# Optimization experiments

Measured on AMD Instinct MI355X. Metric: run time of the kernel, lower is better.

## Reference

```python
import jax, jax.numpy as jnp
import numpy as np

B, F_DIM, T = 16, 256, 4096
L = 128           # latent_dim
CF = 2            # combineVQ_frames
K = 2             # codebook_num
M = 1024          # codebook_size (n_embeddings)
D = L * CF // K   # codebook_dim = 128
TC = T // CF      # combined frames
ALPHA = -5.0      # distance->logit scale
TAU = 2.0         # max_temp (curr_temp at init)


def setup_inputs() -> dict:
    key = jax.random.key(0)
    k1, k2, k3, k4, k5 = jax.random.split(key, 5)
    inputs = jax.random.normal(k1, (B, F_DIM, T, 1), dtype=jnp.float32)
    # xavier-ish scaled 1x1 conv weights
    w1 = jax.random.normal(k2, (L, F_DIM), dtype=jnp.float32) * (2.0 / (L + F_DIM)) ** 0.5
    w2 = jax.random.normal(k3, (F_DIM, L), dtype=jnp.float32) * (2.0 / (L + F_DIM)) ** 0.5
    # codebooks init uniform(-1, 1) as in nn.init.uniform_(a=-1, b=1)
    codebooks = jax.random.uniform(k4, (K, M, D), dtype=jnp.float32, minval=-1.0, maxval=1.0)
    # gumbel noise that torch's F.gumbel_softmax would sample internally
    u = jax.random.uniform(k5, (K, B * TC, M), dtype=jnp.float32, minval=1e-7, maxval=1.0 - 1e-7)
    gumbels = -jnp.log(-jnp.log(u))
    return {"inputs": inputs, "w1": w1, "w2": w2, "codebooks": codebooks, "gumbels": gumbels}


def _vq_layer(vq_in, emb, g):
    # vq_in: [B, TC, D], emb: [M, D], g: [B*TC, M]
    xf = vq_in.reshape(-1, D)  # [N, D]
    dist = (jnp.sum(emb ** 2, axis=1)[None, :]
            + jnp.sum(xf ** 2, axis=1, keepdims=True)
            - 2.0 * (xf @ emb.T))                      # [N, M]
    logits = ALPHA * dist
    # straight-through hard gumbel-softmax (training path of F.gumbel_softmax(hard=True))
    y_soft = jax.nn.softmax((logits + g) / TAU, axis=-1)
    idx = jnp.argmax(y_soft, axis=-1)                  # [N]
    y_hard = jax.nn.one_hot(idx, M, dtype=y_soft.dtype)
    y = y_hard + y_soft - jax.lax.stop_gradient(y_soft)
    q = y @ emb                                        # [N, D] dequantize
    return q.reshape(B, TC, D), idx.reshape(B, TC)


def reference(inputs, w1, w2, codebooks, gumbels):
    # conv1x1_1: [B, F, T, 1] -> [B, L, T, 1]; then squeeze(-1).permute(0,2,1) -> [B, T, L]
    x = jnp.einsum('bfto,lf->btl', inputs, w1)         # [B, T, L]
    # combine frames and split channels across codebooks
    xc = x.reshape(B, TC, CF, L)                       # [B, TC, CF, L]
    chunks = jnp.split(xc, K, axis=-1)                 # K x [B, TC, CF, L/K]
    quants, inds = [], []
    for i in range(K):
        vq_in = chunks[i].reshape(B, TC, D)            # CF*(L/K) == D
        q, idx = _vq_layer(vq_in, codebooks[i], gumbels[i])
        quants.append(q.reshape(B, TC, CF, L // K))
        inds.append(idx)
    vq_feat = jnp.concatenate(quants, axis=-1).reshape(B, T, L)  # [B, T, L]
    # conv1x1_2: back to [B, F, T, 1]
    out = jnp.einsum('btl,fl->bft', vq_feat, w2)[..., None]
    quant_inds = jnp.stack(inds, axis=-1)              # [B, TC, K]
    return out, vq_feat, quant_inds
```

## Files before the change

kernel.cpp:

```cpp
#include <hip/hip_runtime.h>
#include <cstdint>
#include <cmath>

#define B_ 16
#define F_ 256
#define T_ 4096
#define L_ 128
#define TC_ 2048
#define D_ 128
#define M_ 1024
#define NROWS_ 32768

#define PAD 132


__global__ __launch_bounds__(256) void gemm1_kernel(
    const float* __restrict__ in, const float* __restrict__ w1,
    float* __restrict__ x) {
  __shared__ float As[32 * PAD];
  __shared__ float Bs[32 * PAD];
  const int tid = threadIdx.x;
  const int blk = blockIdx.x;
  const int b = blk >> 5;
  const int t0 = (blk & 31) << 7;
  const int tm = tid & 15;
  const int tr = tid >> 4;
  const float* inb = in + (size_t)b * F_ * T_;
  float acc[8][8];
#pragma unroll
  for (int i = 0; i < 8; ++i)
#pragma unroll
    for (int j = 0; j < 8; ++j) acc[i][j] = 0.f;

  for (int f0 = 0; f0 < F_; f0 += 32) {
#pragma unroll
    for (int it = 0; it < 4; ++it) {
      int e = tid + it * 256;
      int ff = e >> 5, q = e & 31;
      float4 v = *(const float4*)(inb + (size_t)(f0 + ff) * T_ + t0 + q * 4);
      *(float4*)(&As[ff * PAD + q * 4]) = v;
    }
#pragma unroll
    for (int it = 0; it < 4; ++it) {
      int e = tid + it * 256;
      int l = e >> 3, q = e & 7;
      float4 v = *(const float4*)(w1 + l * F_ + f0 + q * 4);
      Bs[(q * 4 + 0) * PAD + l] = v.x;
      Bs[(q * 4 + 1) * PAD + l] = v.y;
      Bs[(q * 4 + 2) * PAD + l] = v.z;
      Bs[(q * 4 + 3) * PAD + l] = v.w;
    }
    __syncthreads();
#pragma unroll
    for (int ff = 0; ff < 32; ++ff) {
      float a[8], w[8];
      *(float4*)&a[0] = *(const float4*)&As[ff * PAD + tr * 8];
      *(float4*)&a[4] = *(const float4*)&As[ff * PAD + tr * 8 + 4];
      *(float4*)&w[0] = *(const float4*)&Bs[ff * PAD + 4 * tm];
      *(float4*)&w[4] = *(const float4*)&Bs[ff * PAD + 64 + 4 * tm];
#pragma unroll
      for (int i = 0; i < 8; ++i)
#pragma unroll
        for (int j = 0; j < 8; ++j) acc[i][j] = fmaf(a[i], w[j], acc[i][j]);
    }
    __syncthreads();
  }
  float* xb = x + ((size_t)b * T_ + t0) * L_;
#pragma unroll
  for (int i = 0; i < 8; ++i) {
    float* dst = xb + (size_t)(tr * 8 + i) * L_;
    *(float4*)(dst + 4 * tm) = make_float4(acc[i][0], acc[i][1], acc[i][2], acc[i][3]);
    *(float4*)(dst + 64 + 4 * tm) = make_float4(acc[i][4], acc[i][5], acc[i][6], acc[i][7]);
  }
}

__global__ __launch_bounds__(256) void c2_kernel(const float* __restrict__ cbs,
                                                 float* __restrict__ c2) {
  int m = blockIdx.x * 256 + threadIdx.x;
  const float* row = cbs + (size_t)m * D_;
  float s = 0.f;
#pragma unroll
  for (int d = 0; d < D_; d += 4) {
    float4 v = *(const float4*)(row + d);
    s += v.x * v.x;
    s += v.y * v.y;
    s += v.z * v.z;
    s += v.w * v.w;
  }
  c2[m] = s;
}

__global__ __launch_bounds__(256) void vq_kernel(
    const float* __restrict__ x, const float* __restrict__ cbs,
    const float* __restrict__ gum, const float* __restrict__ c2,
    float* __restrict__ vq_feat, float* __restrict__ qinds) {
  __shared__ float smem[2 * 32 * PAD];
  __shared__ int widx[128];
  float* Xs = smem;
  float* Es = smem + 32 * PAD;
  const int tid = threadIdx.x;
  const int blk = blockIdx.x;
  const int cb = blk >> 8;
  const int n0 = (blk & 255) << 7;
  const int tm = tid & 15;
  const int tr = tid >> 4;
  const float* cbp = cbs + (size_t)cb * M_ * D_;
  const float* gp = gum + (size_t)cb * NROWS_ * M_;
  const float* c2p = c2 + cb * M_;

  float best[8];
  int bidx[8];
#pragma unroll
  for (int i = 0; i < 8; ++i) {
    best[i] = -INFINITY;
    bidx[i] = 0;
  }

  for (int mt = 0; mt < 8; ++mt) {
    const int m0 = mt << 7;
    float acc[8][8];
#pragma unroll
    for (int i = 0; i < 8; ++i)
#pragma unroll
      for (int j = 0; j < 8; ++j) acc[i][j] = 0.f;

    for (int d0 = 0; d0 < D_; d0 += 32) {
      const int cf = d0 >> 6;
      const int j0 = d0 & 63;
#pragma unroll
      for (int it = 0; it < 4; ++it) {
        int e = tid + it * 256;
        int r = e >> 3, q = e & 7;
        int n = n0 + r;
        int bb = n >> 11, tc = n & 2047;
        const float* src =
            x + ((size_t)bb * T_ + 2 * tc + cf) * L_ + cb * 64 + j0 + q * 4;
        float4 v = *(const float4*)src;
        Xs[(q * 4 + 0) * PAD + r] = v.x;
        Xs[(q * 4 + 1) * PAD + r] = v.y;
        Xs[(q * 4 + 2) * PAD + r] = v.z;
        Xs[(q * 4 + 3) * PAD + r] = v.w;
      }
#pragma unroll
      for (int it = 0; it < 4; ++it) {
        int e = tid + it * 256;
        int mm = e >> 3, q = e & 7;
        const float* src = cbp + (size_t)(m0 + mm) * D_ + d0 + q * 4;
        float4 v = *(const float4*)src;
        Es[(q * 4 + 0) * PAD + mm] = v.x;
        Es[(q * 4 + 1) * PAD + mm] = v.y;
        Es[(q * 4 + 2) * PAD + mm] = v.z;
        Es[(q * 4 + 3) * PAD + mm] = v.w;
      }
      __syncthreads();
#pragma unroll
      for (int dd = 0; dd < 32; ++dd) {
        float a[8], w[8];
        *(float4*)&a[0] = *(const float4*)&Xs[dd * PAD + tr * 8];
        *(float4*)&a[4] = *(const float4*)&Xs[dd * PAD + tr * 8 + 4];
        *(float4*)&w[0] = *(const float4*)&Es[dd * PAD + 4 * tm];
        *(float4*)&w[4] = *(const float4*)&Es[dd * PAD + 64 + 4 * tm];
#pragma unroll
        for (int i = 0; i < 8; ++i)
#pragma unroll
          for (int j = 0; j < 8; ++j) acc[i][j] = fmaf(a[i], w[j], acc[i][j]);
      }
      __syncthreads();
    }
    float cc[8];
    *(float4*)&cc[0] = *(const float4*)(c2p + m0 + 4 * tm);
    *(float4*)&cc[4] = *(const float4*)(c2p + m0 + 64 + 4 * tm);
#pragma unroll
    for (int i = 0; i < 8; ++i) {
      int n = n0 + tr * 8 + i;
      const float* grow = gp + (size_t)n * M_ + m0;
      float g[8];
      *(float4*)&g[0] = *(const float4*)(grow + 4 * tm);
      *(float4*)&g[4] = *(const float4*)(grow + 64 + 4 * tm);
#pragma unroll
      for (int j = 0; j < 8; ++j) {
        float dist = cc[j] - 2.f * acc[i][j];
        float sc = fmaf(-5.f, dist, g[j]);
        if (sc > best[i]) {
          best[i] = sc;
          bidx[i] = m0 + ((j >> 2) ? (64 + 4 * tm + (j & 3)) : (4 * tm + (j & 3)));
        }
      }
    }
  }
  float* rbest = smem;
  int* ridx = (int*)(smem + 128 * 17);
#pragma unroll
  for (int i = 0; i < 8; ++i) {
    rbest[(tr * 8 + i) * 17 + tm] = best[i];
    ridx[(tr * 8 + i) * 17 + tm] = bidx[i];
  }
  __syncthreads();
  if (tid < 128) {
    float bv = rbest[tid * 17];
    int bi = ridx[tid * 17];
#pragma unroll
    for (int k = 1; k < 16; ++k) {
      float v = rbest[tid * 17 + k];
      int ii = ridx[tid * 17 + k];
      if (v > bv || (v == bv && ii < bi)) {
        bv = v;
        bi = ii;
      }
    }
    widx[tid] = bi;
    int n = n0 + tid;
    qinds[(size_t)n * 2 + cb] = (float)bi;
  }
  __syncthreads();
  const int jj = (tid & 15) * 4;
  for (int seg = tid >> 4; seg < 256; seg += 16) {
    int r = seg >> 1, cf = seg & 1;
    int wi = widx[r];
    float4 v = *(const float4*)(cbp + (size_t)wi * D_ + cf * 64 + jj);
    int n = n0 + r;
    int bb = n >> 11, tc = n & 2047;
    float* dst = vq_feat + ((size_t)bb * T_ + 2 * tc + cf) * L_ + cb * 64 + jj;
    *(float4*)dst = v;
  }
}

__global__ __launch_bounds__(256) void gemm2_kernel(
    const float* __restrict__ vq, const float* __restrict__ w2,
    float* __restrict__ out) {
  __shared__ float As[32 * PAD];
  __shared__ float Bs[32 * PAD];
  const int tid = threadIdx.x;
  const int blk = blockIdx.x;
  const int b = blk >> 6;
  const int rest = blk & 63;
  const int t0 = (rest >> 1) << 7;
  const int f0 = (rest & 1) << 7;
  const int tm = tid & 15;
  const int tr = tid >> 4;
  const float* vb = vq + (size_t)b * T_ * L_;
  float acc[8][8];
#pragma unroll
  for (int i = 0; i < 8; ++i)
#pragma unroll
    for (int j = 0; j < 8; ++j) acc[i][j] = 0.f;

  for (int l0 = 0; l0 < L_; l0 += 32) {
#pragma unroll
    for (int it = 0; it < 4; ++it) {
      int e = tid + it * 256;
      int t = e >> 3, q = e & 7;
      float4 v = *(const float4*)(vb + (size_t)(t0 + t) * L_ + l0 + q * 4);
      As[(q * 4 + 0) * PAD + t] = v.x;
      As[(q * 4 + 1) * PAD + t] = v.y;
      As[(q * 4 + 2) * PAD + t] = v.z;
      As[(q * 4 + 3) * PAD + t] = v.w;
    }
#pragma unroll
    for (int it = 0; it < 4; ++it) {
      int e = tid + it * 256;
      int f = e >> 3, q = e & 7;
      float4 v = *(const float4*)(w2 + (size_t)(f0 + f) * L_ + l0 + q * 4);
      Bs[(q * 4 + 0) * PAD + f] = v.x;
      Bs[(q * 4 + 1) * PAD + f] = v.y;
      Bs[(q * 4 + 2) * PAD + f] = v.z;
      Bs[(q * 4 + 3) * PAD + f] = v.w;
    }
    __syncthreads();
#pragma unroll
    for (int dd = 0; dd < 32; ++dd) {
      float a[8], w[8];
      *(float4*)&a[0] = *(const float4*)&As[dd * PAD + tr * 8];
      *(float4*)&a[4] = *(const float4*)&As[dd * PAD + tr * 8 + 4];
      *(float4*)&w[0] = *(const float4*)&Bs[dd * PAD + 4 * tm];
      *(float4*)&w[4] = *(const float4*)&Bs[dd * PAD + 64 + 4 * tm];
#pragma unroll
      for (int i = 0; i < 8; ++i)
#pragma unroll
        for (int j = 0; j < 8; ++j) acc[i][j] = fmaf(a[i], w[j], acc[i][j]);
    }
    __syncthreads();
  }
  float* ob = out + ((size_t)b * F_ + f0) * T_ + t0;
#pragma unroll
  for (int jj = 0; jj < 4; ++jj) {
    float* dst = ob + (size_t)(4 * tm + jj) * T_ + tr * 8;
    *(float4*)dst = make_float4(acc[0][jj], acc[1][jj], acc[2][jj], acc[3][jj]);
    *(float4*)(dst + 4) = make_float4(acc[4][jj], acc[5][jj], acc[6][jj], acc[7][jj]);
    float* dst2 = ob + (size_t)(64 + 4 * tm + jj) * T_ + tr * 8;
    *(float4*)dst2 =
        make_float4(acc[0][4 + jj], acc[1][4 + jj], acc[2][4 + jj], acc[3][4 + jj]);
    *(float4*)(dst2 + 4) =
        make_float4(acc[4][4 + jj], acc[5][4 + jj], acc[6][4 + jj], acc[7][4 + jj]);
  }
}

extern "C" void kernel_launch(void* const* d_in, const int* in_sizes, int n_in,
                              void* d_out, int out_size, void* d_ws,
                              size_t ws_size, hipStream_t stream) {
  const float* in = (const float*)d_in[0];
  const float* w1 = (const float*)d_in[1];
  const float* w2 = (const float*)d_in[2];
  const float* cbs = (const float*)d_in[3];
  const float* gum = (const float*)d_in[4];
  float* out = (float*)d_out;
  float* vq_feat = out + 16777216;
  float* qinds = out + 25165824;
  float* x = out;
  float* c2 = out + 8388608;

  hipLaunchKernelGGL(gemm1_kernel, dim3(512), dim3(256), 0, stream, in, w1, x);
  hipLaunchKernelGGL(c2_kernel, dim3(8), dim3(256), 0, stream, cbs, c2);
  hipLaunchKernelGGL(vq_kernel, dim3(512), dim3(256), 0, stream, x, cbs, gum,
                     c2, vq_feat, qinds);
  hipLaunchKernelGGL(gemm2_kernel, dim3(1024), dim3(256), 0, stream, vq_feat,
                     w2, out);
}
```

Before: 684.6 us.

## Halve row tiles to 64 and keep full X tile resident in shared memory

All three GEMM-style kernels move from 128-row to 64-row tiles with 4x8 per-thread accumulators, which doubles the grid size and cuts register pressure so more waves can be resident on the 256 CUs. The VQ kernel also loads its entire 64x128 X slice into shared memory once, instead of reloading X for every codebook tile. The cost is lower arithmetic intensity per thread and more repeated loads of codebook tiles across blocks, since each block now covers fewer rows.

```diff
diff --git a/kernel.cpp b/kernel.cpp
--- a/kernel.cpp
+++ b/kernel.cpp
@@ -11,55 +11,54 @@
 #define M_ 1024
 #define NROWS_ 32768
 
-#define PAD 132
+#define PADE 132
 
 
 __global__ __launch_bounds__(256) void gemm1_kernel(
     const float* __restrict__ in, const float* __restrict__ w1,
     float* __restrict__ x) {
-  __shared__ float As[32 * PAD];
-  __shared__ float Bs[32 * PAD];
+  __shared__ float As[32 * 64];
+  __shared__ float Bs[32 * PADE];
   const int tid = threadIdx.x;
   const int blk = blockIdx.x;
-  const int b = blk >> 5;
-  const int t0 = (blk & 31) << 7;
+  const int b = blk >> 6;
+  const int t0 = (blk & 63) << 6;
   const int tm = tid & 15;
   const int tr = tid >> 4;
   const float* inb = in + (size_t)b * F_ * T_;
-  float acc[8][8];
-#pragma unroll
-  for (int i = 0; i < 8; ++i)
+  float acc[4][8];
+#pragma unroll
+  for (int i = 0; i < 4; ++i)
 #pragma unroll
     for (int j = 0; j < 8; ++j) acc[i][j] = 0.f;
 
   for (int f0 = 0; f0 < F_; f0 += 32) {
 #pragma unroll
-    for (int it = 0; it < 4; ++it) {
+    for (int it = 0; it < 2; ++it) {
       int e = tid + it * 256;
-      int ff = e >> 5, q = e & 31;
+      int ff = e >> 4, q = e & 15;
       float4 v = *(const float4*)(inb + (size_t)(f0 + ff) * T_ + t0 + q * 4);
-      *(float4*)(&As[ff * PAD + q * 4]) = v;
+      *(float4*)(&As[ff * 64 + q * 4]) = v;
     }
 #pragma unroll
     for (int it = 0; it < 4; ++it) {
       int e = tid + it * 256;
       int l = e >> 3, q = e & 7;
       float4 v = *(const float4*)(w1 + l * F_ + f0 + q * 4);
-      Bs[(q * 4 + 0) * PAD + l] = v.x;
-      Bs[(q * 4 + 1) * PAD + l] = v.y;
-      Bs[(q * 4 + 2) * PAD + l] = v.z;
-      Bs[(q * 4 + 3) * PAD + l] = v.w;
+      Bs[(q * 4 + 0) * PADE + l] = v.x;
+      Bs[(q * 4 + 1) * PADE + l] = v.y;
+      Bs[(q * 4 + 2) * PADE + l] = v.z;
+      Bs[(q * 4 + 3) * PADE + l] = v.w;
     }
     __syncthreads();
 #pragma unroll
     for (int ff = 0; ff < 32; ++ff) {
-      float a[8], w[8];
-      *(float4*)&a[0] = *(const float4*)&As[ff * PAD + tr * 8];
-      *(float4*)&a[4] = *(const float4*)&As[ff * PAD + tr * 8 + 4];
-      *(float4*)&w[0] = *(const float4*)&Bs[ff * PAD + 4 * tm];
-      *(float4*)&w[4] = *(const float4*)&Bs[ff * PAD + 64 + 4 * tm];
-#pragma unroll
-      for (int i = 0; i < 8; ++i)
+      float a[4], w[8];
+      *(float4*)&a[0] = *(const float4*)&As[ff * 64 + tr * 4];
+      *(float4*)&w[0] = *(const float4*)&Bs[ff * PADE + 4 * tm];
+      *(float4*)&w[4] = *(const float4*)&Bs[ff * PADE + 64 + 4 * tm];
+#pragma unroll
+      for (int i = 0; i < 4; ++i)
 #pragma unroll
         for (int j = 0; j < 8; ++j) acc[i][j] = fmaf(a[i], w[j], acc[i][j]);
     }
@@ -67,8 +66,8 @@
   }
   float* xb = x + ((size_t)b * T_ + t0) * L_;
 #pragma unroll
-  for (int i = 0; i < 8; ++i) {
-    float* dst = xb + (size_t)(tr * 8 + i) * L_;
+  for (int i = 0; i < 4; ++i) {
+    float* dst = xb + (size_t)(tr * 4 + i) * L_;
     *(float4*)(dst + 4 * tm) = make_float4(acc[i][0], acc[i][1], acc[i][2], acc[i][3]);
     *(float4*)(dst + 64 + 4 * tm) = make_float4(acc[i][4], acc[i][5], acc[i][6], acc[i][7]);
   }
@@ -94,74 +93,74 @@
     const float* __restrict__ x, const float* __restrict__ cbs,
     const float* __restrict__ gum, const float* __restrict__ c2,
     float* __restrict__ vq_feat, float* __restrict__ qinds) {
-  __shared__ float smem[2 * 32 * PAD];
-  __shared__ int widx[128];
+  __shared__ float smem[128 * 64 + 32 * PADE];
+  __shared__ int widx[64];
   float* Xs = smem;
-  float* Es = smem + 32 * PAD;
+  float* Es = smem + 128 * 64;
   const int tid = threadIdx.x;
   const int blk = blockIdx.x;
-  const int cb = blk >> 8;
-  const int n0 = (blk & 255) << 7;
+  const int cb = blk >> 9;
+  const int n0 = (blk & 511) << 6;
   const int tm = tid & 15;
   const int tr = tid >> 4;
   const float* cbp = cbs + (size_t)cb * M_ * D_;
   const float* gp = gum + (size_t)cb * NROWS_ * M_;
   const float* c2p = c2 + cb * M_;
 
-  float best[8];
-  int bidx[8];
-#pragma unroll
-  for (int i = 0; i < 8; ++i) {
+#pragma unroll
+  for (int it = 0; it < 8; ++it) {
+    int e = tid + it * 256;
+    int r = e & 63, qq = e >> 6;
+    int n = n0 + r;
+    int bb = n >> 11, tc = n & 2047;
+    int d = qq * 4;
+    int cf = d >> 6, j = d & 63;
+    const float* src = x + ((size_t)bb * T_ + 2 * tc + cf) * L_ + cb * 64 + j;
+    float4 v = *(const float4*)src;
+    Xs[(d + 0) * 64 + r] = v.x;
+    Xs[(d + 1) * 64 + r] = v.y;
+    Xs[(d + 2) * 64 + r] = v.z;
+    Xs[(d + 3) * 64 + r] = v.w;
+  }
+  __syncthreads();
+
+  float best[4];
+  int bidx[4];
+#pragma unroll
+  for (int i = 0; i < 4; ++i) {
     best[i] = -INFINITY;
     bidx[i] = 0;
   }
 
   for (int mt = 0; mt < 8; ++mt) {
     const int m0 = mt << 7;
-    float acc[8][8];
-#pragma unroll
-    for (int i = 0; i < 8; ++i)
+    float acc[4][8];
+#pragma unroll
+    for (int i = 0; i < 4; ++i)
 #pragma unroll
       for (int j = 0; j < 8; ++j) acc[i][j] = 0.f;
 
     for (int d0 = 0; d0 < D_; d0 += 32) {
-      const int cf = d0 >> 6;
-      const int j0 = d0 & 63;
-#pragma unroll
-      for (int it = 0; it < 4; ++it) {
-        int e = tid + it * 256;
-        int r = e >> 3, q = e & 7;
-        int n = n0 + r;
-        int bb = n >> 11, tc = n & 2047;
-        const float* src =
-            x + ((size_t)bb * T_ + 2 * tc + cf) * L_ + cb * 64 + j0 + q * 4;
-        float4 v = *(const float4*)src;
-        Xs[(q * 4 + 0) * PAD + r] = v.x;
-        Xs[(q * 4 + 1) * PAD + r] = v.y;
-        Xs[(q * 4 + 2) * PAD + r] = v.z;
-        Xs[(q * 4 + 3) * PAD + r] = v.w;
-      }
 #pragma unroll
       for (int it = 0; it < 4; ++it) {
         int e = tid + it * 256;
         int mm = e >> 3, q = e & 7;
         const float* src = cbp + (size_t)(m0 + mm) * D_ + d0 + q * 4;
         float4 v = *(const float4*)src;
-        Es[(q * 4 + 0) * PAD + mm] = v.x;
-        Es[(q * 4 + 1) * PAD + mm] = v.y;
-        Es[(q * 4 + 2) * PAD + mm] = v.z;
-        Es[(q * 4 + 3) * PAD + mm] = v.w;
+        Es[(q * 4 + 0) * PADE + mm] = v.x;
+        Es[(q * 4 + 1) * PADE + mm] = v.y;
+        Es[(q * 4 + 2) * PADE + mm] = v.z;
+        Es[(q * 4 + 3) * PADE + mm] = v.w;
       }
       __syncthreads();
 #pragma unroll
       for (int dd = 0; dd < 32; ++dd) {
-        float a[8], w[8];
-        *(float4*)&a[0] = *(const float4*)&Xs[dd * PAD + tr * 8];
-        *(float4*)&a[4] = *(const float4*)&Xs[dd * PAD + tr * 8 + 4];
-        *(float4*)&w[0] = *(const float4*)&Es[dd * PAD + 4 * tm];
-        *(float4*)&w[4] = *(const float4*)&Es[dd * PAD + 64 + 4 * tm];
-#pragma unroll
-        for (int i = 0; i < 8; ++i)
+        float a[4], w[8];
+        *(float4*)&a[0] = *(const float4*)&Xs[(d0 + dd) * 64 + tr * 4];
+        *(float4*)&w[0] = *(const float4*)&Es[dd * PADE + 4 * tm];
+        *(float4*)&w[4] = *(const float4*)&Es[dd * PADE + 64 + 4 * tm];
+#pragma unroll
+        for (int i = 0; i < 4; ++i)
 #pragma unroll
           for (int j = 0; j < 8; ++j) acc[i][j] = fmaf(a[i], w[j], acc[i][j]);
       }
@@ -171,8 +170,8 @@
     *(float4*)&cc[0] = *(const float4*)(c2p + m0 + 4 * tm);
     *(float4*)&cc[4] = *(const float4*)(c2p + m0 + 64 + 4 * tm);
 #pragma unroll
-    for (int i = 0; i < 8; ++i) {
-      int n = n0 + tr * 8 + i;
+    for (int i = 0; i < 4; ++i) {
+      int n = n0 + tr * 4 + i;
       const float* grow = gp + (size_t)n * M_ + m0;
       float g[8];
       *(float4*)&g[0] = *(const float4*)(grow + 4 * tm);
@@ -189,14 +188,14 @@
     }
   }
   float* rbest = smem;
-  int* ridx = (int*)(smem + 128 * 17);
-#pragma unroll
-  for (int i = 0; i < 8; ++i) {
-    rbest[(tr * 8 + i) * 17 + tm] = best[i];
-    ridx[(tr * 8 + i) * 17 + tm] = bidx[i];
+  int* ridx = (int*)(smem + 64 * 17);
+#pragma unroll
+  for (int i = 0; i < 4; ++i) {
+    rbest[(tr * 4 + i) * 17 + tm] = best[i];
+    ridx[(tr * 4 + i) * 17 + tm] = bidx[i];
   }
   __syncthreads();
-  if (tid < 128) {
+  if (tid < 64) {
     float bv = rbest[tid * 17];
     int bi = ridx[tid * 17];
 #pragma unroll
@@ -214,7 +213,7 @@
   }
   __syncthreads();
   const int jj = (tid & 15) * 4;
-  for (int seg = tid >> 4; seg < 256; seg += 16) {
+  for (int seg = tid >> 4; seg < 128; seg += 16) {
     int r = seg >> 1, cf = seg & 1;
     int wi = widx[r];
     float4 v = *(const float4*)(cbp + (size_t)wi * D_ + cf * 64 + jj);
@@ -228,54 +227,53 @@
 __global__ __launch_bounds__(256) void gemm2_kernel(
     const float* __restrict__ vq, const float* __restrict__ w2,
     float* __restrict__ out) {
-  __shared__ float As[32 * PAD];
-  __shared__ float Bs[32 * PAD];
+  __shared__ float As[32 * 68];
+  __shared__ float Bs[32 * PADE];
   const int tid = threadIdx.x;
   const int blk = blockIdx.x;
-  const int b = blk >> 6;
-  const int rest = blk & 63;
-  const int t0 = (rest >> 1) << 7;
+  const int b = blk >> 7;
+  const int rest = blk & 127;
+  const int t0 = (rest >> 1) << 6;
   const int f0 = (rest & 1) << 7;
   const int tm = tid & 15;
   const int tr = tid >> 4;
   const float* vb = vq + (size_t)b * T_ * L_;
-  float acc[8][8];
-#pragma unroll
-  for (int i = 0; i < 8; ++i)
+  float acc[4][8];
+#pragma unroll
+  for (int i = 0; i < 4; ++i)
 #pragma unroll
     for (int j = 0; j < 8; ++j) acc[i][j] = 0.f;
 
   for (int l0 = 0; l0 < L_; l0 += 32) {
 #pragma unroll
-    for (int it = 0; it < 4; ++it) {
+    for (int it = 0; it < 2; ++it) {
       int e = tid + it * 256;
       int t = e >> 3, q = e & 7;
       float4 v = *(const float4*)(vb + (size_t)(t0 + t) * L_ + l0 + q * 4);
-      As[(q * 4 + 0) * PAD + t] = v.x;
-      As[(q * 4 + 1) * PAD + t] = v.y;
-      As[(q * 4 + 2) * PAD + t] = v.z;
-      As[(q * 4 + 3) * PAD + t] = v.w;
+      As[(q * 4 + 0) * 68 + t] = v.x;
+      As[(q * 4 + 1) * 68 + t] = v.y;
+      As[(q * 4 + 2) * 68 + t] = v.z;
+      As[(q * 4 + 3) * 68 + t] = v.w;
     }
 #pragma unroll
     for (int it = 0; it < 4; ++it) {
       int e = tid + it * 256;
       int f = e >> 3, q = e & 7;
       float4 v = *(const float4*)(w2 + (size_t)(f0 + f) * L_ + l0 + q * 4);
-      Bs[(q * 4 + 0) * PAD + f] = v.x;
-      Bs[(q * 4 + 1) * PAD + f] = v.y;
-      Bs[(q * 4 + 2) * PAD + f] = v.z;
-      Bs[(q * 4 + 3) * PAD + f] = v.w;
+      Bs[(q * 4 + 0) * PADE + f] = v.x;
+      Bs[(q * 4 + 1) * PADE + f] = v.y;
+      Bs[(q * 4 + 2) * PADE + f] = v.z;
+      Bs[(q * 4 + 3) * PADE + f] = v.w;
     }
     __syncthreads();
 #pragma unroll
     for (int dd = 0; dd < 32; ++dd) {
-      float a[8], w[8];
-      *(float4*)&a[0] = *(const float4*)&As[dd * PAD + tr * 8];
-      *(float4*)&a[4] = *(const float4*)&As[dd * PAD + tr * 8 + 4];
-      *(float4*)&w[0] = *(const float4*)&Bs[dd * PAD + 4 * tm];
-      *(float4*)&w[4] = *(const float4*)&Bs[dd * PAD + 64 + 4 * tm];
-#pragma unroll
-      for (int i = 0; i < 8; ++i)
+      float a[4], w[8];
+      *(float4*)&a[0] = *(const float4*)&As[dd * 68 + tr * 4];
+      *(float4*)&w[0] = *(const float4*)&Bs[dd * PADE + 4 * tm];
+      *(float4*)&w[4] = *(const float4*)&Bs[dd * PADE + 64 + 4 * tm];
+#pragma unroll
+      for (int i = 0; i < 4; ++i)
 #pragma unroll
         for (int j = 0; j < 8; ++j) acc[i][j] = fmaf(a[i], w[j], acc[i][j]);
     }
@@ -284,14 +282,10 @@
   float* ob = out + ((size_t)b * F_ + f0) * T_ + t0;
 #pragma unroll
   for (int jj = 0; jj < 4; ++jj) {
-    float* dst = ob + (size_t)(4 * tm + jj) * T_ + tr * 8;
-    *(float4*)dst = make_float4(acc[0][jj], acc[1][jj], acc[2][jj], acc[3][jj]);
-    *(float4*)(dst + 4) = make_float4(acc[4][jj], acc[5][jj], acc[6][jj], acc[7][jj]);
-    float* dst2 = ob + (size_t)(64 + 4 * tm + jj) * T_ + tr * 8;
-    *(float4*)dst2 =
+    *(float4*)(ob + (size_t)(4 * tm + jj) * T_ + tr * 4) =
+        make_float4(acc[0][jj], acc[1][jj], acc[2][jj], acc[3][jj]);
+    *(float4*)(ob + (size_t)(64 + 4 * tm + jj) * T_ + tr * 4) =
         make_float4(acc[0][4 + jj], acc[1][4 + jj], acc[2][4 + jj], acc[3][4 + jj]);
-    *(float4*)(dst2 + 4) =
-        make_float4(acc[4][4 + jj], acc[5][4 + jj], acc[6][4 + jj], acc[7][4 + jj]);
   }
 }
 
@@ -309,10 +303,10 @@
   float* x = out;
   float* c2 = out + 8388608;
 
-  hipLaunchKernelGGL(gemm1_kernel, dim3(512), dim3(256), 0, stream, in, w1, x);
+  hipLaunchKernelGGL(gemm1_kernel, dim3(1024), dim3(256), 0, stream, in, w1, x);
   hipLaunchKernelGGL(c2_kernel, dim3(8), dim3(256), 0, stream, cbs, c2);
-  hipLaunchKernelGGL(vq_kernel, dim3(512), dim3(256), 0, stream, x, cbs, gum,
+  hipLaunchKernelGGL(vq_kernel, dim3(1024), dim3(256), 0, stream, x, cbs, gum,
                      c2, vq_feat, qinds);
-  hipLaunchKernelGGL(gemm2_kernel, dim3(1024), dim3(256), 0, stream, vq_feat,
+  hipLaunchKernelGGL(gemm2_kernel, dim3(2048), dim3(256), 0, stream, vq_feat,
                      w2, out);
 }
```

New measurement: 693.5 us. About the same (+1.3%).
